# Kernel optimization log

Hardware: AMD Instinct MI355X
Metric: run time of the kernel (lower is better)

## Reference

```python
import jax, jax.numpy as jnp
import numpy as np

B, H, T, D = 4, 8, 8192, 64
NUM_CLUSTERS = 64
WINDOW_SIZE = 128
COMMITMENT = 1e-4
TOKEN_SELF_ATTN_VALUE = -50000.0
EPS = 1e-5


def l2norm(x, axis=-1):
    return x / jnp.linalg.norm(x, axis=axis, keepdims=True).clip(1e-12)


def shift(x):
    # relative->absolute position shift; x: (..., i, j) with i == j == wsz
    *lead, i, j = x.shape
    zero_pad = jnp.zeros((*lead, i, i), dtype=x.dtype)
    x = jnp.concatenate([x, zero_pad], axis=-1)          # (..., i, j+i)
    l = i + j - 1
    x = x.reshape(*lead, i * (i + j))
    pad = (-x.shape[-1]) % l
    if pad:
        x = jnp.concatenate([x, jnp.zeros((*lead, pad), dtype=x.dtype)], axis=-1)
    x = x.reshape(*lead, -1, l)
    return x[..., :i, i - 1:]


def setup_inputs() -> dict:
    key = jax.random.key(0)
    k1, k2, k3, k4 = jax.random.split(key, 4)
    qk = jax.random.normal(k1, (B, H, T, D), dtype=jnp.float32)
    v = jax.random.normal(k2, (B, H, T, D), dtype=jnp.float32)
    means = jax.random.normal(k3, (H, NUM_CLUSTERS, D), dtype=jnp.float32)
    rel_weights = jax.random.normal(k4, (WINDOW_SIZE, H, D), dtype=jnp.float32)
    return {"qk": qk, "v": v, "means": means, "rel_weights": rel_weights}


def reference(qk, v, means, rel_weights):
    b, h, t, d = qk.shape
    wsz = min(WINDOW_SIZE, t)
    nc = NUM_CLUSTERS
    scale = d ** -0.5

    # --- kmeans routing (eval: no iterations, fixed means) ---
    k_routing = l2norm(qk)                                        # bhtd
    means_ng = jax.lax.stop_gradient(means)
    dists = jnp.einsum('bhld,hcd->bhlc', jax.lax.stop_gradient(k_routing), means_ng)
    buckets = jnp.argmax(dists, axis=-1)                          # bht
    # top-wsz tokens per cluster, sorted by position
    _, topk_idx = jax.lax.top_k(dists.transpose(0, 1, 3, 2), wsz)  # bhc,wsz
    indices = jnp.sort(topk_idx, axis=-1).reshape(b, h, nc * wsz)  # bhN

    # commitment loss (grad flows only through k_routing, means is a buffer)
    routed_means = means_ng[jnp.arange(h)[None, :, None], buckets]  # bhtd
    commitment_loss = jnp.mean((k_routing - routed_means) ** 2) * COMMITMENT

    # --- gather tokens per cluster ---
    qk_g = jnp.take_along_axis(qk, indices[..., None], axis=2).reshape(b, h, nc, wsz, d)
    v_g = jnp.take_along_axis(v, indices[..., None], axis=2).reshape(b, h, nc, wsz, d)

    q = qk_g
    k = l2norm(qk_g)
    dots = jnp.einsum('bhnid,bhnjd->bhnij', q, k) * scale

    # relative positional bias
    rel = jnp.einsum('bhnid,jhd->bhnij', q, rel_weights) * scale
    dots = dots + shift(rel)

    # mask self-attention on the diagonal
    eye = jnp.eye(wsz, dtype=bool)
    dots = jnp.where(eye, TOKEN_SELF_ATTN_VALUE, dots)

    attn = jax.nn.softmax(dots, axis=-1)
    bo = jnp.einsum('bhnij,bhnjd->bhnid', attn, v_g)
    so = bo.reshape(b, h, nc * wsz, d)

    # --- scatter-mean back to sequence positions ---
    N = nc * wsz
    flat_idx = (jnp.arange(b * h)[:, None] * t + indices.reshape(b * h, N)).reshape(-1)
    so_flat = so.reshape(b * h * N, d)
    numer = jax.ops.segment_sum(so_flat, flat_idx, num_segments=b * h * t)
    denom = jax.ops.segment_sum(jnp.ones((b * h * N,), so.dtype), flat_idx, num_segments=b * h * t)
    out = (numer / (denom[:, None] + EPS)).reshape(b, h, t, d)

    return out, commitment_loss
```

## Files before the change

kernel.cpp:

```cpp
#include <hip/hip_runtime.h>
#include <math.h>

typedef _Float16 h16;
typedef _Float16 f16x8 __attribute__((ext_vector_type(8)));
typedef float f32x4 __attribute__((ext_vector_type(4)));

#define Bc 4
#define Hc 8
#define Tc 8192
#define Dc 64
#define NCc 64
#define WSZc 128
#define BHc (Bc*Hc)
#define MAXPc 16
#define OVFCAP 4095
#define OUT_ELEMS (16777216u)

#define MFMA16(a,b,c) __builtin_amdgcn_mfma_f32_16x16x32_f16(a,b,c,0,0,0)

__global__ __launch_bounds__(256) void k_dists(const float* __restrict__ qk,
                                               const float* __restrict__ means,
                                               float* __restrict__ dists,
                                               float* __restrict__ loss_acc) {
    __shared__ float sm[NCc*Dc];
    __shared__ float red[4];
    int tid = threadIdx.x;
    int blk = blockIdx.x;
    int bh  = blk >> 5;
    int chunk = blk & 31;
    int h = bh & (Hc-1);

    const float* mh = means + (size_t)h*NCc*Dc;
    for (int i = tid; i < NCc*Dc; i += 256) sm[i] = mh[i];
    __syncthreads();

    int t = chunk*256 + tid;
    const float* qrow = qk + ((size_t)bh*Tc + t)*Dc;
    float q[Dc];
    #pragma unroll
    for (int d = 0; d < Dc; d += 4) {
        float4 f = *(const float4*)(qrow + d);
        q[d] = f.x; q[d+1] = f.y; q[d+2] = f.z; q[d+3] = f.w;
    }
    float n2 = 0.f;
    #pragma unroll
    for (int d = 0; d < Dc; d++) n2 += q[d]*q[d];
    float nrm = sqrtf(n2);
    if (nrm < 1e-12f) nrm = 1e-12f;
    float inv = 1.0f/nrm;

    float best = -3.4e38f; int bc = 0;
    float* dbase = dists + ((size_t)bh*NCc)*Tc + (size_t)chunk*256 + tid;
    for (int c = 0; c < NCc; c++) {
        float acc = 0.f;
        const float* mc = sm + c*Dc;
        #pragma unroll
        for (int d = 0; d < Dc; d++) acc += q[d]*mc[d];
        float dv = acc*inv;
        dbase[(size_t)c*Tc] = dv;
        if (dv > best) { best = dv; bc = c; }
    }
    float ls = 0.f;
    const float* mb = sm + bc*Dc;
    #pragma unroll
    for (int d = 0; d < Dc; d++) {
        float diff = q[d]*inv - mb[d];
        ls += diff*diff;
    }
    float lf = ls;
    #pragma unroll
    for (int o = 32; o >= 1; o >>= 1) lf += __shfl_down(lf, o, 64);
    if ((tid & 63) == 0) red[tid >> 6] = lf;
    __syncthreads();
    if (tid == 0) atomicAdd(loss_acc, red[0]+red[1]+red[2]+red[3]);
}

__device__ inline unsigned blockScanIncl(unsigned v, volatile unsigned* wsum,
                                         int lane, int wid, unsigned* ptotal) {
    unsigned x = v;
    #pragma unroll
    for (int s = 1; s < 64; s <<= 1) {
        unsigned o = __shfl_up(x, s, 64);
        if (lane >= s) x += o;
    }
    if (lane == 63) wsum[wid] = x;
    __syncthreads();
    unsigned off = 0, tot = 0;
    #pragma unroll
    for (int w2 = 0; w2 < 4; w2++) {
        unsigned s2 = wsum[w2];
        if (w2 < wid) off += s2;
        tot += s2;
    }
    *ptotal = tot;
    return x + off;
}

__global__ __launch_bounds__(256, 4) void k_topk(const float* __restrict__ dists,
                                              int* __restrict__ indices,
                                              unsigned* __restrict__ cnt,
                                              unsigned short* __restrict__ slots,
                                              unsigned* __restrict__ aux) {
    __shared__ unsigned hist[4096];
    __shared__ unsigned bmap[256];
    __shared__ unsigned eqbuf[256];
    __shared__ unsigned wsum[4];
    __shared__ unsigned sh_prefix;
    __shared__ int      sh_k, cnt_eq;

    int tid = threadIdx.x;
    int lane = tid & 63, wid = tid >> 6;
    int bhc = blockIdx.x, bh = bhc >> 6, c = bhc & 63;
    const float* dp = dists + (size_t)bhc*Tc;

    for (int i = tid; i < 4096; i += 256) hist[i] = 0u;
    if (tid == 0) { sh_k = WSZc; sh_prefix = 0u; cnt_eq = 0; }
    bmap[tid] = 0u;
    __syncthreads();

    unsigned key[8][4];
    #pragma unroll
    for (int ch = 0; ch < 8; ch++) {
        float4 f = *(const float4*)(dp + ch*1024 + tid*4);
        float fv[4] = {f.x, f.y, f.z, f.w};
        #pragma unroll
        for (int j = 0; j < 4; j++) {
            unsigned u = __float_as_uint(fv[j]);
            u = (u & 0x80000000u) ? ~u : (u | 0x80000000u);
            key[ch][j] = u;
            atomicAdd(&hist[u >> 20], 1u);
        }
    }
    __syncthreads();

    unsigned prefix = 0u; int k = WSZc;
    #pragma unroll
    for (int lvl = 0; lvl < 3; lvl++) {
        const int shift   = (lvl == 0) ? 20 : (lvl == 1 ? 8 : 0);
        const int nper    = (lvl == 2) ? 1 : 16;
        const unsigned nbm = (lvl == 2) ? 255u : 4095u;
        if (lvl > 0) {
            const unsigned maskH = (lvl == 1) ? 0xFFF00000u : 0xFFFFFF00u;
            for (int i = tid; i <= (int)nbm; i += 256) hist[i] = 0u;
            __syncthreads();
            #pragma unroll
            for (int ch = 0; ch < 8; ch++)
                #pragma unroll
                for (int j = 0; j < 4; j++) {
                    unsigned ky = key[ch][j];
                    if ((ky & maskH) == prefix)
                        atomicAdd(&hist[(ky >> shift) & nbm], 1u);
                }
            __syncthreads();
        }
        int tBase = tid*nper;
        unsigned psum = 0;
        for (int i = 0; i < nper; i++) psum += hist[tBase + i];
        unsigned total;
        unsigned incl = blockScanIncl(psum, wsum, lane, wid, &total);
        unsigned beyond = total - incl;
        unsigned suff   = beyond + psum;
        if (beyond < (unsigned)k && (unsigned)k <= suff) {
            unsigned run = beyond;
            for (int i = nper - 1; i >= 0; i--) {
                unsigned hb = hist[tBase + i];
                run += hb;
                if (run >= (unsigned)k) {
                    sh_prefix = prefix | ((unsigned)(tBase + i) << shift);
                    sh_k = k - (int)(run - hb);
                    break;
                }
            }
        }
        __syncthreads();
        prefix = sh_prefix; k = sh_k;
        __syncthreads();
    }
    unsigned Kthr = prefix;
    int kEq = k;

    #pragma unroll
    for (int ch = 0; ch < 8; ch++)
        #pragma unroll
        for (int j = 0; j < 4; j++) {
            unsigned ky = key[ch][j];
            int t = ch*1024 + tid*4 + j;
            if (ky > Kthr) atomicOr(&bmap[t >> 5], 1u << (t & 31));
            else if (ky == Kthr) {
                int p = atomicAdd(&cnt_eq, 1);
                if (p < 256) eqbuf[p] = (unsigned)t;
            }
        }
    __syncthreads();
    if (cnt_eq == kEq) {
        if (tid < kEq) {
            unsigned t = eqbuf[tid];
            atomicOr(&bmap[t >> 5], 1u << (t & 31));
        }
    } else {
        int ce = cnt_eq < 256 ? cnt_eq : 256;
        if (tid >= ce) eqbuf[tid] = 0xFFFFFFFFu;
        __syncthreads();
        for (int k2 = 2; k2 <= 256; k2 <<= 1) {
            for (int j = k2 >> 1; j >= 1; j >>= 1) {
                int i = tid, ixj = i ^ j;
                if (ixj > i) {
                    bool up = ((i & k2) == 0);
                    unsigned a = eqbuf[i], b = eqbuf[ixj];
                    if ((a > b) == up) { eqbuf[i] = b; eqbuf[ixj] = a; }
                }
                __syncthreads();
            }
        }
        if (tid < kEq) {
            unsigned t = eqbuf[tid];
            atomicOr(&bmap[t >> 5], 1u << (t & 31));
        }
    }
    __syncthreads();

    unsigned w = bmap[tid];
    int pc = __popc(w);
    unsigned total2;
    unsigned incl2 = blockScanIncl((unsigned)pc, wsum, lane, wid, &total2);
    int pos = (int)(incl2 - pc);
    while (w) {
        int b = __ffs(w) - 1; w &= w - 1;
        int t = tid*32 + b;
        indices[(size_t)bhc*WSZc + pos] = t;
        unsigned row = ((unsigned)bh << 13) + (unsigned)t;
        unsigned p2 = atomicAdd(&cnt[row], 1u);
        if (p2 < MAXPc) slots[(size_t)row*MAXPc + p2] = (unsigned short)(c*128 + pos);
        else {
            unsigned o = atomicAdd(&aux[0], 1u);
            if (o < OVFCAP) aux[2+o] = (unsigned)(bhc*WSZc + pos);
        }
        pos++;
    }
}

__global__ __launch_bounds__(256, 2) void k_attn(const float* __restrict__ qk,
                                                 const float* __restrict__ v,
                                                 const float* __restrict__ relw,
                                                 const int* __restrict__ indices,
                                                 float* __restrict__ bo) {
    __shared__ __align__(16) h16 qf[128*72];
    __shared__ __align__(16) h16 uv[128*72];
    __shared__ __align__(16) h16 pt[128*136];
    __shared__ int   sidx[128];
    __shared__ float sinv[128];

    int tid = threadIdx.x;
    int bhc = blockIdx.x, bh = bhc >> 6, h = bh & (Hc-1);
    int lane = tid & 63, wid = tid >> 6;
    int quad = lane >> 4, lj = lane & 15;
    int i0 = wid*32;

    for (int i = tid; i < 128*136/2; i += 256) ((unsigned*)pt)[i] = 0u;
    if (tid < 128) sidx[tid] = indices[(size_t)bhc*WSZc + tid];
    __syncthreads();

    {
        int i = tid >> 1, hf = tid & 1;
        const float* qrow = qk   + ((size_t)bh*Tc + sidx[i])*Dc + hf*32;
        const float* wrow = relw + ((size_t)i*Hc + h)*Dc + hf*32;
        float n2 = 0.f;
        #pragma unroll
        for (int k8 = 0; k8 < 4; k8++) {
            float4 a = *(const float4*)(qrow + k8*8);
            float4 b = *(const float4*)(qrow + k8*8 + 4);
            float4 c = *(const float4*)(wrow + k8*8);
            float4 d = *(const float4*)(wrow + k8*8 + 4);
            n2 += a.x*a.x + a.y*a.y + a.z*a.z + a.w*a.w
                + b.x*b.x + b.y*b.y + b.z*b.z + b.w*b.w;
            f16x8 hq = {(h16)a.x,(h16)a.y,(h16)a.z,(h16)a.w,
                        (h16)b.x,(h16)b.y,(h16)b.z,(h16)b.w};
            f16x8 hw = {(h16)c.x,(h16)c.y,(h16)c.z,(h16)c.w,
                        (h16)d.x,(h16)d.y,(h16)d.z,(h16)d.w};
            *(f16x8*)&qf[i*72 + hf*32 + k8*8] = hq;
            *(f16x8*)&uv[i*72 + hf*32 + k8*8] = hw;
        }
        n2 += __shfl_xor(n2, 1, 64);
        if (hf == 0) {
            float nr = sqrtf(n2); if (nr < 1e-12f) nr = 1e-12f;
            sinv[i] = 0.125f / nr;
        }
    }
    __syncthreads();

    {
        f32x4 accR[2][8];
        #pragma unroll
        for (int mt = 0; mt < 2; mt++)
            #pragma unroll
            for (int nt = 0; nt < 8; nt++)
                #pragma unroll
                for (int e = 0; e < 4; e++) accR[mt][nt][e] = 0.f;
        #pragma unroll
        for (int k0 = 0; k0 < 64; k0 += 32) {
            f16x8 a0 = *(const f16x8*)&qf[(i0 + lj)*72 + k0 + quad*8];
            f16x8 a1 = *(const f16x8*)&qf[(i0 + 16 + lj)*72 + k0 + quad*8];
            #pragma unroll
            for (int nt = 0; nt < 8; nt++) {
                f16x8 bf = *(const f16x8*)&uv[(nt*16 + lj)*72 + k0 + quad*8];
                accR[0][nt] = MFMA16(a0, bf, accR[0][nt]);
                accR[1][nt] = MFMA16(a1, bf, accR[1][nt]);
            }
        }
        #pragma unroll
        for (int mt = 0; mt < 2; mt++)
            #pragma unroll
            for (int nt = 0; nt < 8; nt++)
                #pragma unroll
                for (int r = 0; r < 4; r++) {
                    int i = i0 + mt*16 + quad*4 + r;
                    int j = nt*16 + lj - 127 + i;
                    if (j >= 0) pt[i*136 + j] = (h16)(accR[mt][nt][r] * 0.125f);
                }
    }

    float4 vr[8];
    {
        int j = tid >> 1, hf = tid & 1;
        const float* vrow = v + ((size_t)bh*Tc + sidx[j])*Dc + hf*32;
        #pragma unroll
        for (int r = 0; r < 8; r++) vr[r] = *(const float4*)(vrow + r*4);
    }
    __syncthreads();

    f32x4 accS[2][8];
    #pragma unroll
    for (int mt = 0; mt < 2; mt++)
        #pragma unroll
        for (int nt = 0; nt < 8; nt++)
            #pragma unroll
            for (int e = 0; e < 4; e++) accS[mt][nt][e] = 0.f;
    #pragma unroll
    for (int k0 = 0; k0 < 64; k0 += 32) {
        f16x8 a0 = *(const f16x8*)&qf[(i0 + lj)*72 + k0 + quad*8];
        f16x8 a1 = *(const f16x8*)&qf[(i0 + 16 + lj)*72 + k0 + quad*8];
        #pragma unroll
        for (int nt = 0; nt < 8; nt++) {
            f16x8 bf = *(const f16x8*)&qf[(nt*16 + lj)*72 + k0 + quad*8];
            accS[0][nt] = MFMA16(a0, bf, accS[0][nt]);
            accS[1][nt] = MFMA16(a1, bf, accS[1][nt]);
        }
    }
    #pragma unroll
    for (int nt = 0; nt < 8; nt++) {
        int j = nt*16 + lj;
        float sj = sinv[j];
        #pragma unroll
        for (int mt = 0; mt < 2; mt++)
            #pragma unroll
            for (int r = 0; r < 4; r++) {
                int i = i0 + mt*16 + quad*4 + r;
                float s = accS[mt][nt][r]*sj + (float)pt[i*136 + j];
                accS[mt][nt][r] = (i == j) ? -50000.0f : s;
            }
    }
    #pragma unroll
    for (int mt = 0; mt < 2; mt++)
        #pragma unroll
        for (int r = 0; r < 4; r++) {
            float mx = accS[mt][0][r];
            #pragma unroll
            for (int nt = 1; nt < 8; nt++) mx = fmaxf(mx, accS[mt][nt][r]);
            #pragma unroll
            for (int st = 1; st <= 8; st <<= 1) mx = fmaxf(mx, __shfl_xor(mx, st, 64));
            float sum = 0.f;
            #pragma unroll
            for (int nt = 0; nt < 8; nt++) {
                float e = __expf(accS[mt][nt][r] - mx);
                accS[mt][nt][r] = e; sum += e;
            }
            #pragma unroll
            for (int st = 1; st <= 8; st <<= 1) sum += __shfl_xor(sum, st, 64);
            float inv = 1.0f/sum;
            #pragma unroll
            for (int nt = 0; nt < 8; nt++) accS[mt][nt][r] *= inv;
        }
    #pragma unroll
    for (int mt = 0; mt < 2; mt++)
        #pragma unroll
        for (int nt = 0; nt < 8; nt++)
            #pragma unroll
            for (int r = 0; r < 4; r++) {
                int i = i0 + mt*16 + quad*4 + r;
                pt[i*136 + nt*16 + lj] = (h16)accS[mt][nt][r];
            }
    {
        int j = tid >> 1, hf = tid & 1;
        #pragma unroll
        for (int r = 0; r < 8; r++) {
            int d0 = hf*32 + r*4;
            float4 f = vr[r];
            uv[(d0+0)*136 + j] = (h16)f.x;
            uv[(d0+1)*136 + j] = (h16)f.y;
            uv[(d0+2)*136 + j] = (h16)f.z;
            uv[(d0+3)*136 + j] = (h16)f.w;
        }
    }
    __syncthreads();

    f32x4 accO[2][4];
    #pragma unroll
    for (int mt = 0; mt < 2; mt++)
        #pragma unroll
        for (int nt = 0; nt < 4; nt++)
            #pragma unroll
            for (int e = 0; e < 4; e++) accO[mt][nt][e] = 0.f;
    #pragma unroll
    for (int k0 = 0; k0 < 128; k0 += 32) {
        f16x8 a0 = *(const f16x8*)&pt[(i0 + lj)*136 + k0 + quad*8];
        f16x8 a1 = *(const f16x8*)&pt[(i0 + 16 + lj)*136 + k0 + quad*8];
        #pragma unroll
        for (int nt = 0; nt < 4; nt++) {
            f16x8 bf = *(const f16x8*)&uv[(nt*16 + lj)*136 + k0 + quad*8];
            accO[0][nt] = MFMA16(a0, bf, accO[0][nt]);
            accO[1][nt] = MFMA16(a1, bf, accO[1][nt]);
        }
    }
    #pragma unroll
    for (int mt = 0; mt < 2; mt++)
        #pragma unroll
        for (int nt = 0; nt < 4; nt++)
            #pragma unroll
            for (int r = 0; r < 4; r++) {
                int i = i0 + mt*16 + quad*4 + r;
                bo[((size_t)bhc*WSZc + i)*Dc + nt*16 + lj] = accO[mt][nt][r];
            }
}

__global__ __launch_bounds__(256) void k_final(const float* __restrict__ bo,
                                               const unsigned short* __restrict__ slots,
                                               const unsigned* __restrict__ cnt,
                                               const int* __restrict__ indices,
                                               const unsigned* __restrict__ aux,
                                               float* __restrict__ out) {
    int row  = blockIdx.x*4 + (threadIdx.x >> 6);
    int lane = threadIdx.x & 63;
    unsigned c = cnt[row];
    unsigned m = c < MAXPc ? c : MAXPc;
    int bh = row >> 13;
    float acc = 0.f;
    const unsigned short* sl = slots + (size_t)row*MAXPc;
    for (unsigned p = 0; p < m; p++)
        acc += bo[(((size_t)bh << 13) + sl[p])*Dc + lane];
    if (c > MAXPc) {
        unsigned n = aux[0]; if (n > OVFCAP) n = OVFCAP;
        int tok = row & 8191;
        for (unsigned q = 0; q < n; q++) {
            unsigned e = aux[2+q];
            if ((int)(e >> 13) == bh && indices[e] == tok)
                acc += bo[(((size_t)bh << 13) + (e & 8191))*Dc + lane];
        }
    }
    out[(size_t)row*Dc + lane] = acc * (1.0f/((float)c + 1e-5f));
    if (row == 0 && lane == 0)
        out[OUT_ELEMS] = ((const float*)aux)[1] * (float)(1e-4 / 16777216.0);
}

extern "C" void kernel_launch(void* const* d_in, const int* in_sizes, int n_in,
                              void* d_out, int out_size, void* d_ws, size_t ws_size,
                              hipStream_t stream) {
    const float* qk    = (const float*)d_in[0];
    const float* v     = (const float*)d_in[1];
    const float* means = (const float*)d_in[2];
    const float* relw  = (const float*)d_in[3];
    float* out = (float*)d_out;
    char*  ws  = (char*)d_ws;

    size_t off = 0;
    float* dists = (float*)(ws + off);
    float* bo    = dists;
    off += (size_t)BHc*NCc*Tc*4;
    int* indices = (int*)(ws + off); off += (size_t)BHc*NCc*WSZc*4;
    unsigned* cnt = (unsigned*)(ws + off); off += (size_t)BHc*Tc*4;
    unsigned* aux = (unsigned*)(ws + off); off += (size_t)(2+OVFCAP)*4;
    unsigned short* slots = (unsigned short*)(ws + off);
    off += (size_t)BHc*Tc*MAXPc*2;

    hipMemsetAsync(cnt, 0, (size_t)BHc*Tc*4 + (size_t)(2+OVFCAP)*4, stream);

    k_dists <<<BHc*(Tc/256), 256, 0, stream>>>(qk, means, dists, (float*)aux + 1);
    k_topk  <<<BHc*NCc,      256, 0, stream>>>(dists, indices, cnt, slots, aux);
    k_attn  <<<BHc*NCc,      256, 0, stream>>>(qk, v, relw, indices, bo);
    k_final <<<BHc*Tc/4,     256, 0, stream>>>(bo, slots, cnt, indices, aux, out);
}
```

Measured before the change: 353.9 us.

## Shrink attention LDS footprint, skip masked rel tiles, and swizzle block order

The attention kernel merges its q and v staging buffers into one shared array and drops the explicit zeroing of the score buffer. Relative-bias entries above the diagonal are now masked with an index guard instead of being zeroed. Relative weights are read straight from global memory into MFMA operands, and each wave skips the relative-bias tiles that only produce masked positions. Blocks are remapped so neighbouring blocks spread across heads and batches, and the launch bound is raised to three blocks per CU. Together these aim to cut shared-memory use and wasted MFMA work so more blocks fit per CU. The cost is uncoalesced global loads of relw and an extra barrier ordering the buffer reuse.

Result: slower. 401.1 us (+13.3%).

```diff
diff --git a/kernel.cpp b/kernel.cpp
--- a/kernel.cpp
+++ b/kernel.cpp
@@ -239,46 +239,40 @@
     }
 }
 
-__global__ __launch_bounds__(256, 2) void k_attn(const float* __restrict__ qk,
+__global__ __launch_bounds__(256, 3) void k_attn(const float* __restrict__ qk,
                                                  const float* __restrict__ v,
                                                  const float* __restrict__ relw,
                                                  const int* __restrict__ indices,
                                                  float* __restrict__ bo) {
-    __shared__ __align__(16) h16 qf[128*72];
-    __shared__ __align__(16) h16 uv[128*72];
-    __shared__ __align__(16) h16 pt[128*136];
+    __shared__ __align__(16) h16 qv[128*72];
+    __shared__ __align__(16) h16 sp[128*136];
     __shared__ int   sidx[128];
     __shared__ float sinv[128];
 
     int tid = threadIdx.x;
-    int bhc = blockIdx.x, bh = bhc >> 6, h = bh & (Hc-1);
+    int bid = blockIdx.x;
+    int bhc = ((bid & 7) << 8) | (bid >> 3);
+    int bh = bhc >> 6, h = bh & (Hc-1);
     int lane = tid & 63, wid = tid >> 6;
     int quad = lane >> 4, lj = lane & 15;
     int i0 = wid*32;
 
-    for (int i = tid; i < 128*136/2; i += 256) ((unsigned*)pt)[i] = 0u;
     if (tid < 128) sidx[tid] = indices[(size_t)bhc*WSZc + tid];
     __syncthreads();
 
     {
         int i = tid >> 1, hf = tid & 1;
-        const float* qrow = qk   + ((size_t)bh*Tc + sidx[i])*Dc + hf*32;
-        const float* wrow = relw + ((size_t)i*Hc + h)*Dc + hf*32;
+        const float* qrow = qk + ((size_t)bh*Tc + sidx[i])*Dc + hf*32;
         float n2 = 0.f;
         #pragma unroll
         for (int k8 = 0; k8 < 4; k8++) {
             float4 a = *(const float4*)(qrow + k8*8);
             float4 b = *(const float4*)(qrow + k8*8 + 4);
-            float4 c = *(const float4*)(wrow + k8*8);
-            float4 d = *(const float4*)(wrow + k8*8 + 4);
             n2 += a.x*a.x + a.y*a.y + a.z*a.z + a.w*a.w
                 + b.x*b.x + b.y*b.y + b.z*b.z + b.w*b.w;
             f16x8 hq = {(h16)a.x,(h16)a.y,(h16)a.z,(h16)a.w,
                         (h16)b.x,(h16)b.y,(h16)b.z,(h16)b.w};
-            f16x8 hw = {(h16)c.x,(h16)c.y,(h16)c.z,(h16)c.w,
-                        (h16)d.x,(h16)d.y,(h16)d.z,(h16)d.w};
-            *(f16x8*)&qf[i*72 + hf*32 + k8*8] = hq;
-            *(f16x8*)&uv[i*72 + hf*32 + k8*8] = hw;
+            *(f16x8*)&qv[i*72 + hf*32 + k8*8] = hq;
         }
         n2 += __shfl_xor(n2, 1, 64);
         if (hf == 0) {
@@ -288,6 +282,7 @@
     }
     __syncthreads();
 
+    int ntMin = 6 - 2*wid;
     {
         f32x4 accR[2][8];
         #pragma unroll
@@ -296,13 +291,19 @@
             for (int nt = 0; nt < 8; nt++)
                 #pragma unroll
                 for (int e = 0; e < 4; e++) accR[mt][nt][e] = 0.f;
+        const float* wh = relw + (size_t)h*Dc;
         #pragma unroll
         for (int k0 = 0; k0 < 64; k0 += 32) {
-            f16x8 a0 = *(const f16x8*)&qf[(i0 + lj)*72 + k0 + quad*8];
-            f16x8 a1 = *(const f16x8*)&qf[(i0 + 16 + lj)*72 + k0 + quad*8];
+            f16x8 a0 = *(const f16x8*)&qv[(i0 + lj)*72 + k0 + quad*8];
+            f16x8 a1 = *(const f16x8*)&qv[(i0 + 16 + lj)*72 + k0 + quad*8];
             #pragma unroll
             for (int nt = 0; nt < 8; nt++) {
-                f16x8 bf = *(const f16x8*)&uv[(nt*16 + lj)*72 + k0 + quad*8];
+                if (nt < ntMin) continue;
+                const float* wp = wh + (size_t)(nt*16 + lj)*(Hc*Dc) + k0 + quad*8;
+                float4 wa = *(const float4*)wp;
+                float4 wc = *(const float4*)(wp + 4);
+                f16x8 bf = {(h16)wa.x,(h16)wa.y,(h16)wa.z,(h16)wa.w,
+                            (h16)wc.x,(h16)wc.y,(h16)wc.z,(h16)wc.w};
                 accR[0][nt] = MFMA16(a0, bf, accR[0][nt]);
                 accR[1][nt] = MFMA16(a1, bf, accR[1][nt]);
             }
@@ -310,13 +311,15 @@
         #pragma unroll
         for (int mt = 0; mt < 2; mt++)
             #pragma unroll
-            for (int nt = 0; nt < 8; nt++)
+            for (int nt = 0; nt < 8; nt++) {
+                if (nt < ntMin) continue;
                 #pragma unroll
                 for (int r = 0; r < 4; r++) {
                     int i = i0 + mt*16 + quad*4 + r;
                     int j = nt*16 + lj - 127 + i;
-                    if (j >= 0) pt[i*136 + j] = (h16)(accR[mt][nt][r] * 0.125f);
+                    if (j >= 0) sp[i*136 + j] = (h16)(accR[mt][nt][r] * 0.125f);
                 }
+            }
     }
 
     float4 vr[8];
@@ -326,7 +329,6 @@
         #pragma unroll
         for (int r = 0; r < 8; r++) vr[r] = *(const float4*)(vrow + r*4);
     }
-    __syncthreads();
 
     f32x4 accS[2][8];
     #pragma unroll
@@ -337,15 +339,17 @@
             for (int e = 0; e < 4; e++) accS[mt][nt][e] = 0.f;
     #pragma unroll
     for (int k0 = 0; k0 < 64; k0 += 32) {
-        f16x8 a0 = *(const f16x8*)&qf[(i0 + lj)*72 + k0 + quad*8];
-        f16x8 a1 = *(const f16x8*)&qf[(i0 + 16 + lj)*72 + k0 + quad*8];
+        f16x8 a0 = *(const f16x8*)&qv[(i0 + lj)*72 + k0 + quad*8];
+        f16x8 a1 = *(const f16x8*)&qv[(i0 + 16 + lj)*72 + k0 + quad*8];
         #pragma unroll
         for (int nt = 0; nt < 8; nt++) {
-            f16x8 bf = *(const f16x8*)&qf[(nt*16 + lj)*72 + k0 + quad*8];
+            f16x8 bf = *(const f16x8*)&qv[(nt*16 + lj)*72 + k0 + quad*8];
             accS[0][nt] = MFMA16(a0, bf, accS[0][nt]);
             accS[1][nt] = MFMA16(a1, bf, accS[1][nt]);
         }
     }
+    __syncthreads();
+
     #pragma unroll
     for (int nt = 0; nt < 8; nt++) {
         int j = nt*16 + lj;
@@ -355,7 +359,8 @@
             #pragma unroll
             for (int r = 0; r < 4; r++) {
                 int i = i0 + mt*16 + quad*4 + r;
-                float s = accS[mt][nt][r]*sj + (float)pt[i*136 + j];
+                float rl = (j <= i) ? (float)sp[i*136 + j] : 0.f;
+                float s = accS[mt][nt][r]*sj + rl;
                 accS[mt][nt][r] = (i == j) ? -50000.0f : s;
             }
     }
@@ -387,18 +392,19 @@
             #pragma unroll
             for (int r = 0; r < 4; r++) {
                 int i = i0 + mt*16 + quad*4 + r;
-                pt[i*136 + nt*16 + lj] = (h16)accS[mt][nt][r];
+                sp[i*136 + nt*16 + lj] = (h16)accS[mt][nt][r];
             }
     {
+        h16* vt = qv;
         int j = tid >> 1, hf = tid & 1;
         #pragma unroll
         for (int r = 0; r < 8; r++) {
             int d0 = hf*32 + r*4;
             float4 f = vr[r];
-            uv[(d0+0)*136 + j] = (h16)f.x;
-            uv[(d0+1)*136 + j] = (h16)f.y;
-            uv[(d0+2)*136 + j] = (h16)f.z;
-            uv[(d0+3)*136 + j] = (h16)f.w;
+            vt[(d0+0)*136 + j] = (h16)f.x;
+            vt[(d0+1)*136 + j] = (h16)f.y;
+            vt[(d0+2)*136 + j] = (h16)f.z;
+            vt[(d0+3)*136 + j] = (h16)f.w;
         }
     }
     __syncthreads();
@@ -412,11 +418,11 @@
             for (int e = 0; e < 4; e++) accO[mt][nt][e] = 0.f;
     #pragma unroll
     for (int k0 = 0; k0 < 128; k0 += 32) {
-        f16x8 a0 = *(const f16x8*)&pt[(i0 + lj)*136 + k0 + quad*8];
-        f16x8 a1 = *(const f16x8*)&pt[(i0 + 16 + lj)*136 + k0 + quad*8];
+        f16x8 a0 = *(const f16x8*)&sp[(i0 + lj)*136 + k0 + quad*8];
+        f16x8 a1 = *(const f16x8*)&sp[(i0 + 16 + lj)*136 + k0 + quad*8];
         #pragma unroll
         for (int nt = 0; nt < 4; nt++) {
-            f16x8 bf = *(const f16x8*)&uv[(nt*16 + lj)*136 + k0 + quad*8];
+            f16x8 bf = *(const f16x8*)&qv[(nt*16 + lj)*136 + k0 + quad*8];
             accO[0][nt] = MFMA16(a0, bf, accO[0][nt]);
             accO[1][nt] = MFMA16(a1, bf, accO[1][nt]);
         }
```
